# Optimization experiments

Measured on AMD Instinct MI355X. Metric: run time of the kernel, lower is better.

Reference implementation:

```python
import jax, jax.numpy as jnp
import numpy as np

D = 1024
H = 8          # MHA fallback num_heads
DH = D // H
DFF = 4096     # mlp_ratio * hidden_size
EPS = 1e-6


def _ln(x, g, b):
    mu = jnp.mean(x, axis=-1, keepdims=True)
    var = jnp.mean((x - mu) ** 2, axis=-1, keepdims=True)
    return (x - mu) * jax.lax.rsqrt(var + EPS) * g + b


def setup_inputs() -> dict:
    key = jax.random.key(0)
    ks = jax.random.split(key, 16)
    s = 0.02
    return {
        "x": jax.random.normal(ks[0], (8, 1024, D), jnp.float32),
        "c": jax.random.normal(ks[1], (8, D), jnp.float32),
        # Mamba-block (attention fallback) params
        "m_ada_w": jax.random.normal(ks[2], (D, 3 * D), jnp.float32) * s,
        "m_ada_b": jnp.zeros((3 * D,), jnp.float32),
        "m_norm_g": jnp.ones((D,), jnp.float32),
        "m_norm_b": jnp.zeros((D,), jnp.float32),
        "in_proj_w": jax.random.normal(ks[3], (3 * D, D), jnp.float32) * s,
        "in_proj_b": jnp.zeros((3 * D,), jnp.float32),
        "out_proj_w": jax.random.normal(ks[4], (D, D), jnp.float32) * s,
        "out_proj_b": jnp.zeros((D,), jnp.float32),
        # FeedForward-block params
        "f_ada_w": jax.random.normal(ks[5], (D, 3 * D), jnp.float32) * s,
        "f_ada_b": jnp.zeros((3 * D,), jnp.float32),
        "f_norm_g": jnp.ones((D,), jnp.float32),
        "f_norm_b": jnp.zeros((D,), jnp.float32),
        "w1": jax.random.normal(ks[6], (D, DFF), jnp.float32) * s,
        "b1": jnp.zeros((DFF,), jnp.float32),
        "w2": jax.random.normal(ks[7], (DFF, D), jnp.float32) * s,
        "b2": jnp.zeros((D,), jnp.float32),
    }


def reference(x, c, m_ada_w, m_ada_b, m_norm_g, m_norm_b, in_proj_w, in_proj_b,
              out_proj_w, out_proj_b, f_ada_w, f_ada_b, f_norm_g, f_norm_b,
              w1, b1, w2, b2):
    B, N, _ = x.shape
    # ---- MambaBlock (MHA fallback), dropout = identity (eval) ----
    mod = jax.nn.silu(c) @ m_ada_w + m_ada_b              # (B, 3D)
    shift, scale, gate = jnp.split(mod, 3, axis=-1)
    h = _ln(x, m_norm_g, m_norm_b)
    h = h * (1.0 + scale[:, None, :]) + shift[:, None, :]
    qkv = h @ in_proj_w.T + in_proj_b                      # (B, N, 3D)
    q, k, v = jnp.split(qkv, 3, axis=-1)
    q = q.reshape(B, N, H, DH)
    k = k.reshape(B, N, H, DH)
    v = v.reshape(B, N, H, DH)
    scores = jnp.einsum("bqhd,bkhd->bhqk", q, k) / np.sqrt(DH).astype(np.float32)
    attn = jax.nn.softmax(scores, axis=-1)
    o = jnp.einsum("bhqk,bkhd->bqhd", attn, v).reshape(B, N, D)
    o = o @ out_proj_w.T + out_proj_b
    x = x + gate[:, None, :] * o
    # ---- FeedForward block ----
    mod2 = jax.nn.silu(c) @ f_ada_w + f_ada_b
    shift2, scale2, gate2 = jnp.split(mod2, 3, axis=-1)
    h = _ln(x, f_norm_g, f_norm_b)
    h = h * (1.0 + scale2[:, None, :]) + shift2[:, None, :]
    h = jax.nn.gelu(h @ w1 + b1, approximate=False) @ w2 + b2
    return x + gate2[:, None, :] * h
```

## Files before the change

kernel.cpp:

```cpp
#include <hip/hip_runtime.h>

typedef __bf16 bf16x8 __attribute__((ext_vector_type(8)));
typedef float f32x4 __attribute__((ext_vector_type(4)));

__device__ __forceinline__ unsigned short f2bf(float f) {
    unsigned int u = __float_as_uint(f);
    unsigned int r = (u + 0x7FFFu + ((u >> 16) & 1u)) >> 16;
    return (unsigned short)r;
}

__device__ __forceinline__ void gload16(const void* g, void* l) {
    __builtin_amdgcn_global_load_lds(
        (const __attribute__((address_space(1))) unsigned int*)g,
        (__attribute__((address_space(3))) unsigned int*)l, 16, 0, 0);
}

__device__ __forceinline__ void barrier_raw() {
    asm volatile("" ::: "memory");
    __builtin_amdgcn_s_barrier();
    asm volatile("" ::: "memory");
}

__device__ __forceinline__ void vmwait0() {
    asm volatile("s_waitcnt vmcnt(0)" ::: "memory");
}

__device__ __forceinline__ float gelu_fast(float u) {
    float z = 1.595769122f * u + 0.071354816f * u * u * u;
    return u / (1.f + __expf(-z));
}

__global__ __launch_bounds__(256) void f2b4(const float* __restrict__ in,
                                            unsigned short* __restrict__ out) {
    size_t i = ((size_t)blockIdx.x * 256 + threadIdx.x) * 4;
    float4 v = *(const float4*)(in + i);
    ushort4 o;
    o.x = f2bf(v.x); o.y = f2bf(v.y); o.z = f2bf(v.z); o.w = f2bf(v.w);
    *(ushort4*)(out + i) = o;
}

__global__ __launch_bounds__(256) void transpose_f2b(const float* __restrict__ in,
                                                     unsigned short* __restrict__ out,
                                                     int R, int C) {
    __shared__ float tile[32][33];
    int r0 = blockIdx.y * 32, c0 = blockIdx.x * 32;
    int tx = threadIdx.x & 31, ty = threadIdx.x >> 5;
#pragma unroll
    for (int i = 0; i < 4; i++) {
        int r = ty + i * 8;
        tile[r][tx] = in[(size_t)(r0 + r) * C + c0 + tx];
    }
    __syncthreads();
#pragma unroll
    for (int i = 0; i < 4; i++) {
        int r = ty + i * 8;
        out[(size_t)(c0 + r) * R + r0 + tx] = f2bf(tile[tx][r]);
    }
}

__global__ __launch_bounds__(256) void transpose_v(const unsigned short* __restrict__ qkv,
                                                   unsigned short* __restrict__ vt) {
    __shared__ unsigned short tile[32][33];
    int head = blockIdx.z;
    int b = head >> 3;
    int n0 = blockIdx.x * 32, d0 = blockIdx.y * 32;
    int tx = threadIdx.x & 31, ty = threadIdx.x >> 5;
    const unsigned short* src = qkv + (size_t)(b * 1024) * 3072 + 2048 + (head & 7) * 128;
#pragma unroll
    for (int i = 0; i < 4; i++) {
        int n = ty + i * 8;
        tile[n][tx] = src[(size_t)(n0 + n) * 3072 + d0 + tx];
    }
    __syncthreads();
#pragma unroll
    for (int i = 0; i < 4; i++) {
        int d = ty + i * 8;
        vt[((size_t)head * 128 + d0 + d) * 1024 + n0 + tx] = tile[tx][d];
    }
}

__global__ __launch_bounds__(256) void ada_mod_part(const float* __restrict__ c,
                                                    const float* __restrict__ W,
                                                    float* __restrict__ partial) {
    __shared__ float sc[8 * 64];
    int kc = blockIdx.y * 64;
    for (int i = threadIdx.x; i < 512; i += 256) {
        int b = i >> 6, k = i & 63;
        float cv = c[b * 1024 + kc + k];
        sc[i] = cv / (1.f + __expf(-cv));
    }
    __syncthreads();
    int j = blockIdx.x * 256 + threadIdx.x;
    float acc[8] = {0, 0, 0, 0, 0, 0, 0, 0};
    for (int k = 0; k < 64; k++) {
        float w = W[(size_t)(kc + k) * 3072 + j];
#pragma unroll
        for (int b = 0; b < 8; b++) acc[b] += sc[b * 64 + k] * w;
    }
#pragma unroll
    for (int b = 0; b < 8; b++) partial[((size_t)blockIdx.y * 8 + b) * 3072 + j] = acc[b];
}

__global__ __launch_bounds__(256) void ada_reduce(const float* __restrict__ partial,
                                                  const float* __restrict__ bias,
                                                  float* __restrict__ out) {
    int idx = blockIdx.x * 256 + threadIdx.x;
    int b = idx / 3072;
    int jj = idx - b * 3072;
    float s = bias[jj];
#pragma unroll
    for (int ch = 0; ch < 16; ch++) s += partial[((size_t)ch * 8 + b) * 3072 + jj];
    out[idx] = s;
}

__global__ __launch_bounds__(256) void ln_mod_kernel(const float* __restrict__ x,
                                                     const float* __restrict__ gamma,
                                                     const float* __restrict__ beta,
                                                     const float* __restrict__ mods,
                                                     unsigned short* __restrict__ out) {
    int row = blockIdx.x;
    int b = row >> 10;
    float4 v = ((const float4*)(x + (size_t)row * 1024))[threadIdx.x];
    float s = v.x + v.y + v.z + v.w;
    float s2 = v.x * v.x + v.y * v.y + v.z * v.z + v.w * v.w;
#pragma unroll
    for (int d = 1; d < 64; d <<= 1) { s += __shfl_xor(s, d); s2 += __shfl_xor(s2, d); }
    __shared__ float red[8];
    int lane = threadIdx.x & 63, wid = threadIdx.x >> 6;
    if (lane == 0) { red[wid] = s; red[4 + wid] = s2; }
    __syncthreads();
    float S = red[0] + red[1] + red[2] + red[3];
    float S2 = red[4] + red[5] + red[6] + red[7];
    float mu = S * (1.f / 1024.f);
    float var = S2 * (1.f / 1024.f) - mu * mu;
    float rs = rsqrtf(var + 1e-6f);
    const float* mrow = mods + b * 3072;
    int j0 = threadIdx.x * 4;
    float hv[4] = {v.x, v.y, v.z, v.w};
    ushort4 o;
    unsigned short* op = (unsigned short*)&o;
#pragma unroll
    for (int i = 0; i < 4; i++) {
        int j = j0 + i;
        float hh = (hv[i] - mu) * rs * gamma[j] + beta[j];
        hh = hh * (1.f + mrow[1024 + j]) + mrow[j];
        op[i] = f2bf(hh);
    }
    *(ushort4*)(out + (size_t)row * 1024 + j0) = o;
}

template <int NF, int EP>
__global__ __launch_bounds__(512, 2) void gemm256(const unsigned short* __restrict__ A,
                                                  const unsigned short* __restrict__ Bt,
                                                  int N, int K, int nx,
                                                  const float* __restrict__ bias,
                                                  const float* __restrict__ xres,
                                                  const float* __restrict__ mods,
                                                  float* __restrict__ outf,
                                                  unsigned short* __restrict__ outb) {
    constexpr int BROWS = NF * 64;
    extern __shared__ __align__(16) char smem[];
    __bf16* AsB = (__bf16*)smem;
    __bf16* BsB = AsB + 2 * 256 * 64;

    int tid = threadIdx.x, lane = tid & 63, wid = tid >> 6;
    int wr = wid >> 2, wc = wid & 3;
    int t = lane & 15, g = lane >> 4;
    int xk = (t & 7) * 8;

    int nwg = gridDim.x;
    int chunk = nwg >> 3;
    int swz = (blockIdx.x & 7) * chunk + (blockIdx.x >> 3);
    int bx = swz % nx, by = swz / nx;
    int rowA0 = by * 256, colB0 = bx * BROWS;

    int rin = tid >> 3;
    int cblk = tid & 7;
    int scol = (cblk ^ (rin & 7)) * 8;

    auto stageA = [&](int nb, int half, int kt1) {
        int k0 = kt1 << 6;
        int r0 = half * 128 + rin;
        gload16(A + (size_t)(rowA0 + r0) * K + k0 + scol,
                (void*)(AsB + nb * (256 * 64) + r0 * 64 + cblk * 8));
        int r1 = r0 + 64;
        gload16(A + (size_t)(rowA0 + r1) * K + k0 + scol,
                (void*)(AsB + nb * (256 * 64) + r1 * 64 + cblk * 8));
    };
    auto stageB4 = [&](int nb, int half, int kt1) {
        int k0 = kt1 << 6;
        int r0 = half * 128 + rin;
        gload16(Bt + (size_t)(colB0 + r0) * K + k0 + scol,
                (void*)(BsB + nb * (BROWS * 64) + r0 * 64 + cblk * 8));
        int r1 = r0 + 64;
        gload16(Bt + (size_t)(colB0 + r1) * K + k0 + scol,
                (void*)(BsB + nb * (BROWS * 64) + r1 * 64 + cblk * 8));
    };
    auto stageB2 = [&](int nb, int half, int kt1) {
        int k0 = kt1 << 6;
        int r0 = half * 64 + rin;
        gload16(Bt + (size_t)(colB0 + r0) * K + k0 + scol,
                (void*)(BsB + nb * (BROWS * 64) + r0 * 64 + cblk * 8));
    };

    f32x4 acc[8][NF];
#pragma unroll
    for (int m = 0; m < 8; m++)
#pragma unroll
        for (int n = 0; n < NF; n++) acc[m][n] = (f32x4){0.f, 0.f, 0.f, 0.f};

    stageA(0, 0, 0); stageA(0, 1, 0);
    if constexpr (NF == 4) { stageB4(0, 0, 0); stageB4(0, 1, 0); }
    else                   { stageB2(0, 0, 0); stageB2(0, 1, 0); }
    vmwait0();
    barrier_raw();

    int NT = K >> 6;
#pragma unroll 1
    for (int kt = 0; kt < NT; ++kt) {
        const __bf16* Ac = AsB + (kt & 1) * (256 * 64);
        const __bf16* Bc = BsB + (kt & 1) * (BROWS * 64);
        int nb = (kt & 1) ^ 1;
        bool more = (kt + 1) < NT;

        auto LDA = [&](int m, int ks) -> bf16x8 {
            return *(const bf16x8*)(Ac + (wr * 128 + m * 16 + t) * 64 + ((ks * 32 + g * 8) ^ xk));
        };
        auto LDB = [&](int n, int ks) -> bf16x8 {
            return *(const bf16x8*)(Bc + (wc * (NF * 16) + n * 16 + t) * 64 + ((ks * 32 + g * 8) ^ xk));
        };

        if constexpr (NF == 4) {
            bf16x8 aF[4][2], bLo[2][2], bHi[2][2];
#pragma unroll
            for (int m = 0; m < 4; m++) { aF[m][0] = LDA(m, 0); aF[m][1] = LDA(m, 1); }
#pragma unroll
            for (int n = 0; n < 2; n++) { bLo[n][0] = LDB(n, 0); bLo[n][1] = LDB(n, 1); }
            if (more) stageA(nb, 0, kt + 1);
            barrier_raw();
            __builtin_amdgcn_s_setprio(1);
#pragma unroll
            for (int m = 0; m < 4; m++)
#pragma unroll
                for (int n = 0; n < 2; n++)
#pragma unroll
                    for (int ks = 0; ks < 2; ks++)
                        acc[m][n] = __builtin_amdgcn_mfma_f32_16x16x32_bf16(aF[m][ks], bLo[n][ks], acc[m][n], 0, 0, 0);
            __builtin_amdgcn_s_setprio(0);
            barrier_raw();
#pragma unroll
            for (int n = 0; n < 2; n++) { bHi[n][0] = LDB(n + 2, 0); bHi[n][1] = LDB(n + 2, 1); }
            if (more) stageA(nb, 1, kt + 1);
            barrier_raw();
            __builtin_amdgcn_s_setprio(1);
#pragma unroll
            for (int m = 0; m < 4; m++)
#pragma unroll
                for (int n = 0; n < 2; n++)
#pragma unroll
                    for (int ks = 0; ks < 2; ks++)
                        acc[m][n + 2] = __builtin_amdgcn_mfma_f32_16x16x32_bf16(aF[m][ks], bHi[n][ks], acc[m][n + 2], 0, 0, 0);
            __builtin_amdgcn_s_setprio(0);
            barrier_raw();
            bf16x8 aH[4][2];
#pragma unroll
            for (int m = 0; m < 4; m++) { aH[m][0] = LDA(m + 4, 0); aH[m][1] = LDA(m + 4, 1); }
            if (more) stageB4(nb, 0, kt + 1);
            barrier_raw();
            __builtin_amdgcn_s_setprio(1);
#pragma unroll
            for (int m = 0; m < 4; m++)
#pragma unroll
                for (int n = 0; n < 2; n++)
#pragma unroll
                    for (int ks = 0; ks < 2; ks++)
                        acc[m + 4][n + 2] = __builtin_amdgcn_mfma_f32_16x16x32_bf16(aH[m][ks], bHi[n][ks], acc[m + 4][n + 2], 0, 0, 0);
            __builtin_amdgcn_s_setprio(0);
            barrier_raw();
            if (more) stageB4(nb, 1, kt + 1);
            __builtin_amdgcn_s_setprio(1);
#pragma unroll
            for (int m = 0; m < 4; m++)
#pragma unroll
                for (int n = 0; n < 2; n++)
#pragma unroll
                    for (int ks = 0; ks < 2; ks++)
                        acc[m + 4][n] = __builtin_amdgcn_mfma_f32_16x16x32_bf16(aH[m][ks], bLo[n][ks], acc[m + 4][n], 0, 0, 0);
            __builtin_amdgcn_s_setprio(0);
            vmwait0();
            barrier_raw();
        } else {
            bf16x8 aF[4][2], bF[2][2];
#pragma unroll
            for (int m = 0; m < 4; m++) { aF[m][0] = LDA(m, 0); aF[m][1] = LDA(m, 1); }
#pragma unroll
            for (int n = 0; n < 2; n++) { bF[n][0] = LDB(n, 0); bF[n][1] = LDB(n, 1); }
            if (more) { stageA(nb, 0, kt + 1); stageB2(nb, 0, kt + 1); }
            barrier_raw();
            __builtin_amdgcn_s_setprio(1);
#pragma unroll
            for (int m = 0; m < 4; m++)
#pragma unroll
                for (int n = 0; n < 2; n++)
#pragma unroll
                    for (int ks = 0; ks < 2; ks++)
                        acc[m][n] = __builtin_amdgcn_mfma_f32_16x16x32_bf16(aF[m][ks], bF[n][ks], acc[m][n], 0, 0, 0);
            __builtin_amdgcn_s_setprio(0);
            barrier_raw();
            bf16x8 aH[4][2];
#pragma unroll
            for (int m = 0; m < 4; m++) { aH[m][0] = LDA(m + 4, 0); aH[m][1] = LDA(m + 4, 1); }
            if (more) { stageA(nb, 1, kt + 1); stageB2(nb, 1, kt + 1); }
            barrier_raw();
            __builtin_amdgcn_s_setprio(1);
#pragma unroll
            for (int m = 0; m < 4; m++)
#pragma unroll
                for (int n = 0; n < 2; n++)
#pragma unroll
                    for (int ks = 0; ks < 2; ks++)
                        acc[m + 4][n] = __builtin_amdgcn_mfma_f32_16x16x32_bf16(aH[m][ks], bF[n][ks], acc[m + 4][n], 0, 0, 0);
            __builtin_amdgcn_s_setprio(0);
            vmwait0();
            barrier_raw();
        }
    }

    int row0 = rowA0 + wr * 128, col0 = colB0 + wc * (NF * 16);
#pragma unroll
    for (int m = 0; m < 8; m++)
#pragma unroll
        for (int n = 0; n < NF; n++) {
            int col = col0 + n * 16 + t;
#pragma unroll
            for (int r = 0; r < 4; r++) {
                int row = row0 + m * 16 + g * 4 + r;
                float v = acc[m][n][r];
                if (EP == 0) {
                    outb[(size_t)row * N + col] = f2bf(v + bias[col]);
                } else if (EP == 1) {
                    int bb = row >> 10;
                    float gt = mods[bb * 3072 + 2048 + col];
                    outf[(size_t)row * 1024 + col] =
                        xres[(size_t)row * 1024 + col] + gt * (v + bias[col]);
                } else if (EP == 2) {
                    outb[(size_t)row * N + col] = f2bf(gelu_fast(v + bias[col]));
                } else {
                    int bb = row >> 10;
                    float gt = mods[bb * 3072 + 2048 + col];
                    outf[(size_t)row * 1024 + col] += gt * (v + bias[col]);
                }
            }
        }
}

__global__ __launch_bounds__(256) void attn_kernel(const unsigned short* __restrict__ qkv,
                                                   const unsigned short* __restrict__ vt,
                                                   unsigned short* __restrict__ o) {
    __shared__ __align__(16) __bf16 Ks[64 * 128];
    __shared__ __align__(16) __bf16 Vts[128 * 64];
    __shared__ __align__(16) __bf16 Pl[4][16][72];
    int bid = blockIdx.x;
    int logical = (bid & 7) * 128 + (bid >> 3);
    int q0 = (logical & 15) * 64;
    int bh = logical >> 4;
    int b = bh >> 3, h = bh & 7;
    int tid = threadIdx.x, lane = tid & 63, w = tid >> 6;
    int t = lane & 15, g = lane >> 4;
    int swzt = (t & 7) << 4;

    const unsigned short* qbase = qkv + (size_t)(b * 1024) * 3072 + h * 128;
    int qrow = q0 + w * 16 + t;
    bf16x8 qf[4];
#pragma unroll
    for (int ks = 0; ks < 4; ks++)
        qf[ks] = *(const bf16x8*)(qbase + (size_t)qrow * 3072 + ks * 32 + g * 8);

    f32x4 Oa[8];
#pragma unroll
    for (int n = 0; n < 8; n++) Oa[n] = (f32x4){0.f, 0.f, 0.f, 0.f};
    float m_r[4] = {-1e30f, -1e30f, -1e30f, -1e30f};
    float l_r[4] = {0.f, 0.f, 0.f, 0.f};
    const float scale = 0.08838834764831845f;

    int krow = tid >> 4;
    int ksrc = (((tid & 15) * 16) ^ ((krow & 7) << 4)) >> 1;
    int vrow = tid >> 3;
    int vsrc = (((tid & 7) * 16) ^ ((vrow & 7) << 4)) >> 1;
    const unsigned short* vtg = vt + (size_t)bh * 128 * 1024;

    for (int kv0 = 0; kv0 < 1024; kv0 += 64) {
        const unsigned short* kb = qkv + (size_t)(b * 1024 + kv0) * 3072 + 1024 + h * 128;
#pragma unroll
        for (int cc = 0; cc < 4; cc++) {
            gload16(kb + (size_t)(cc * 16 + krow) * 3072 + ksrc, (void*)&Ks[cc * 2048 + tid * 8]);
            gload16(vtg + (size_t)(cc * 32 + vrow) * 1024 + kv0 + vsrc, (void*)&Vts[cc * 2048 + tid * 8]);
        }
        __syncthreads();

        f32x4 Sa[4];
#pragma unroll
        for (int n = 0; n < 4; n++) Sa[n] = (f32x4){0.f, 0.f, 0.f, 0.f};
#pragma unroll
        for (int ks = 0; ks < 4; ks++) {
#pragma unroll
            for (int n = 0; n < 4; n++) {
                bf16x8 kf = *(const bf16x8*)&Ks[(n * 16 + t) * 128 + (((ks * 64 + g * 16) ^ swzt) >> 1)];
                Sa[n] = __builtin_amdgcn_mfma_f32_16x16x32_bf16(qf[ks], kf, Sa[n], 0, 0, 0);
            }
        }
#pragma unroll
        for (int r = 0; r < 4; r++) {
            float mx = fmaxf(fmaxf(Sa[0][r], Sa[1][r]), fmaxf(Sa[2][r], Sa[3][r])) * scale;
#pragma unroll
            for (int d = 1; d < 16; d <<= 1) mx = fmaxf(mx, __shfl_xor(mx, d));
            float mn = fmaxf(m_r[r], mx);
            float alpha = __expf(m_r[r] - mn);
            m_r[r] = mn;
            float rs = 0.f;
#pragma unroll
            for (int n = 0; n < 4; n++) {
                float p = __expf(Sa[n][r] * scale - mn);
                Pl[w][g * 4 + r][n * 16 + t] = (__bf16)p;
                rs += p;
            }
#pragma unroll
            for (int d = 1; d < 16; d <<= 1) rs += __shfl_xor(rs, d);
            l_r[r] = l_r[r] * alpha + rs;
#pragma unroll
            for (int n2 = 0; n2 < 8; n2++) Oa[n2][r] *= alpha;
        }
#pragma unroll
        for (int ks2 = 0; ks2 < 2; ks2++) {
            bf16x8 pa = *(const bf16x8*)&Pl[w][t][ks2 * 32 + g * 8];
#pragma unroll
            for (int n2 = 0; n2 < 8; n2++) {
                bf16x8 vf = *(const bf16x8*)&Vts[(n2 * 16 + t) * 64 + (((ks2 * 64 + g * 16) ^ swzt) >> 1)];
                Oa[n2] = __builtin_amdgcn_mfma_f32_16x16x32_bf16(pa, vf, Oa[n2], 0, 0, 0);
            }
        }
        __syncthreads();
    }

#pragma unroll
    for (int r = 0; r < 4; r++) {
        float inv = 1.f / l_r[r];
        int orow = q0 + w * 16 + g * 4 + r;
#pragma unroll
        for (int n2 = 0; n2 < 8; n2++)
            o[(size_t)(b * 1024 + orow) * 1024 + h * 128 + n2 * 16 + t] = f2bf(Oa[n2][r] * inv);
    }
}

extern "C" void kernel_launch(void* const* d_in, const int* in_sizes, int n_in,
                              void* d_out, int out_size, void* d_ws, size_t ws_size,
                              hipStream_t stream) {
    const float* x          = (const float*)d_in[0];
    const float* c          = (const float*)d_in[1];
    const float* m_ada_w    = (const float*)d_in[2];
    const float* m_ada_b    = (const float*)d_in[3];
    const float* m_norm_g   = (const float*)d_in[4];
    const float* m_norm_b   = (const float*)d_in[5];
    const float* in_proj_w  = (const float*)d_in[6];
    const float* in_proj_b  = (const float*)d_in[7];
    const float* out_proj_w = (const float*)d_in[8];
    const float* out_proj_b = (const float*)d_in[9];
    const float* f_ada_w    = (const float*)d_in[10];
    const float* f_ada_b    = (const float*)d_in[11];
    const float* f_norm_g   = (const float*)d_in[12];
    const float* f_norm_b   = (const float*)d_in[13];
    const float* w1         = (const float*)d_in[14];
    const float* b1         = (const float*)d_in[15];
    const float* w2         = (const float*)d_in[16];
    const float* b2         = (const float*)d_in[17];
    float* out = (float*)d_out;
    char* ws = (char*)d_ws;

    unsigned short* Wq   = (unsigned short*)(ws + 0);
    unsigned short* Wo   = (unsigned short*)(ws + 6291456);
    unsigned short* vt   = (unsigned short*)(ws + 8388608);
    unsigned short* W1t  = (unsigned short*)(ws + 8388608);
    unsigned short* W2t  = (unsigned short*)(ws + 16777216);
    float*          modm = (float*)(ws + 25165824);
    float*          modf = (float*)(ws + 25264128);
    unsigned short* hbuf = (unsigned short*)(ws + 25362432);
    float*          part = (float*)(ws + 25362432);
    float*          part2= (float*)(ws + 25362432 + 2097152);
    unsigned short* qkv  = (unsigned short*)(ws + 42139648);
    unsigned short* obuf = (unsigned short*)(ws + 92471296);
    unsigned short* h2   = (unsigned short*)(ws + 42139648);

    hipFuncSetAttribute((const void*)&gemm256<4, 0>, hipFuncAttributeMaxDynamicSharedMemorySize, 131072);
    hipFuncSetAttribute((const void*)&gemm256<4, 2>, hipFuncAttributeMaxDynamicSharedMemorySize, 131072);
    hipFuncSetAttribute((const void*)&gemm256<2, 1>, hipFuncAttributeMaxDynamicSharedMemorySize, 98304);
    hipFuncSetAttribute((const void*)&gemm256<2, 3>, hipFuncAttributeMaxDynamicSharedMemorySize, 98304);

    hipLaunchKernelGGL(ada_mod_part, dim3(12, 16), dim3(256), 0, stream, c, m_ada_w, part);
    hipLaunchKernelGGL(ada_mod_part, dim3(12, 16), dim3(256), 0, stream, c, f_ada_w, part2);
    hipLaunchKernelGGL(ada_reduce, dim3(96), dim3(256), 0, stream, part, m_ada_b, modm);
    hipLaunchKernelGGL(ada_reduce, dim3(96), dim3(256), 0, stream, part2, f_ada_b, modf);

    hipLaunchKernelGGL(f2b4, dim3(3072), dim3(256), 0, stream, in_proj_w, Wq);
    hipLaunchKernelGGL(f2b4, dim3(1024), dim3(256), 0, stream, out_proj_w, Wo);

    hipLaunchKernelGGL(ln_mod_kernel, dim3(8192), dim3(256), 0, stream, x, m_norm_g, m_norm_b, modm, hbuf);
    hipLaunchKernelGGL(HIP_KERNEL_NAME(gemm256<4, 0>), dim3(384), dim3(512), 131072, stream,
                       hbuf, Wq, 3072, 1024, 12, in_proj_b, (const float*)nullptr,
                       (const float*)nullptr, (float*)nullptr, qkv);
    hipLaunchKernelGGL(transpose_v, dim3(32, 4, 64), dim3(256), 0, stream, qkv, vt);
    hipLaunchKernelGGL(attn_kernel, dim3(1024), dim3(256), 0, stream, qkv, vt, obuf);
    hipLaunchKernelGGL(HIP_KERNEL_NAME(gemm256<2, 1>), dim3(256), dim3(512), 98304, stream,
                       obuf, Wo, 1024, 1024, 8, out_proj_b, x, modm, out, (unsigned short*)nullptr);

    hipLaunchKernelGGL(transpose_f2b, dim3(128, 32), dim3(256), 0, stream, w1, W1t, 1024, 4096);
    hipLaunchKernelGGL(transpose_f2b, dim3(32, 128), dim3(256), 0, stream, w2, W2t, 4096, 1024);

    hipLaunchKernelGGL(ln_mod_kernel, dim3(8192), dim3(256), 0, stream, out, f_norm_g, f_norm_b, modf, hbuf);
    hipLaunchKernelGGL(HIP_KERNEL_NAME(gemm256<4, 2>), dim3(512), dim3(512), 131072, stream,
                       hbuf, W1t, 4096, 1024, 16, b1, (const float*)nullptr,
                       (const float*)nullptr, (float*)nullptr, h2);
    hipLaunchKernelGGL(HIP_KERNEL_NAME(gemm256<2, 3>), dim3(256), dim3(512), 98304, stream,
                       h2, W2t, 1024, 4096, 8, b2, (const float*)nullptr, modf, out,
                       (unsigned short*)nullptr);
}
```

Baseline: 434.1 us.

## Double-buffer attention K/V tiles and keep P in registers via transposed S

The attention kernel now uses 512-thread blocks covering 128 query rows, with double-buffered K/V tiles in dynamic shared memory, so the next tile's global-to-LDS loads overlap the current tile's compute. S is computed transposed (K as the A operand), which lets each lane own one query column and do its softmax reduction with two cross-group shuffles. P is converted to the MFMA A-operand layout through lane shuffles instead of a round trip through the LDS P buffer. MFMA sections are wrapped in s_setprio hints. In exchange it doubles LDS per block and adds extra shuffle and select traffic in the inner loop.

New measurement: 392.7 us. -9.5%, faster.

```diff
diff --git a/kernel.cpp b/kernel.cpp
--- a/kernel.cpp
+++ b/kernel.cpp
@@ -354,16 +354,17 @@
         }
 }
 
-__global__ __launch_bounds__(256) void attn_kernel(const unsigned short* __restrict__ qkv,
-                                                   const unsigned short* __restrict__ vt,
-                                                   unsigned short* __restrict__ o) {
-    __shared__ __align__(16) __bf16 Ks[64 * 128];
-    __shared__ __align__(16) __bf16 Vts[128 * 64];
-    __shared__ __align__(16) __bf16 Pl[4][16][72];
+__global__ __launch_bounds__(512, 4) void attn_kernel(const unsigned short* __restrict__ qkv,
+                                                      const unsigned short* __restrict__ vt,
+                                                      unsigned short* __restrict__ o) {
+    extern __shared__ __align__(16) char asmem[];
+    __bf16* Ks = (__bf16*)asmem;
+    __bf16* Vts = Ks + 2 * 64 * 128;
+
     int bid = blockIdx.x;
-    int logical = (bid & 7) * 128 + (bid >> 3);
-    int q0 = (logical & 15) * 64;
-    int bh = logical >> 4;
+    int logical = (bid & 7) * 64 + (bid >> 3);
+    int q0 = (logical & 7) * 128;
+    int bh = logical >> 3;
     int b = bh >> 3, h = bh & 7;
     int tid = threadIdx.x, lane = tid & 63, w = tid >> 6;
     int t = lane & 15, g = lane >> 4;
@@ -379,8 +380,7 @@
     f32x4 Oa[8];
 #pragma unroll
     for (int n = 0; n < 8; n++) Oa[n] = (f32x4){0.f, 0.f, 0.f, 0.f};
-    float m_r[4] = {-1e30f, -1e30f, -1e30f, -1e30f};
-    float l_r[4] = {0.f, 0.f, 0.f, 0.f};
+    float m_r = -1e30f, l_r = 0.f;
     const float scale = 0.08838834764831845f;
 
     int krow = tid >> 4;
@@ -389,62 +389,115 @@
     int vsrc = (((tid & 7) * 16) ^ ((vrow & 7) << 4)) >> 1;
     const unsigned short* vtg = vt + (size_t)bh * 128 * 1024;
 
-    for (int kv0 = 0; kv0 < 1024; kv0 += 64) {
+    auto stage = [&](int buf, int kv0) {
         const unsigned short* kb = qkv + (size_t)(b * 1024 + kv0) * 3072 + 1024 + h * 128;
 #pragma unroll
-        for (int cc = 0; cc < 4; cc++) {
-            gload16(kb + (size_t)(cc * 16 + krow) * 3072 + ksrc, (void*)&Ks[cc * 2048 + tid * 8]);
-            gload16(vtg + (size_t)(cc * 32 + vrow) * 1024 + kv0 + vsrc, (void*)&Vts[cc * 2048 + tid * 8]);
-        }
-        __syncthreads();
-
-        f32x4 Sa[4];
-#pragma unroll
-        for (int n = 0; n < 4; n++) Sa[n] = (f32x4){0.f, 0.f, 0.f, 0.f};
+        for (int cc = 0; cc < 2; cc++) {
+            gload16(kb + (size_t)(cc * 32 + krow) * 3072 + ksrc,
+                    (void*)(Ks + buf * 8192 + cc * 4096 + tid * 8));
+            gload16(vtg + (size_t)(cc * 64 + vrow) * 1024 + kv0 + vsrc,
+                    (void*)(Vts + buf * 8192 + cc * 4096 + tid * 8));
+        }
+    };
+
+    stage(0, 0);
+    vmwait0();
+    barrier_raw();
+
+#pragma unroll 1
+    for (int tile = 0; tile < 16; ++tile) {
+        int cur = tile & 1;
+        bool more = tile < 15;
+        if (more) stage(cur ^ 1, (tile + 1) * 64);
+        const __bf16* Kc = Ks + cur * 8192;
+        const __bf16* Vc = Vts + cur * 8192;
+
+        f32x4 St[4];
+#pragma unroll
+        for (int n = 0; n < 4; n++) St[n] = (f32x4){0.f, 0.f, 0.f, 0.f};
+        __builtin_amdgcn_s_setprio(1);
 #pragma unroll
         for (int ks = 0; ks < 4; ks++) {
 #pragma unroll
             for (int n = 0; n < 4; n++) {
-                bf16x8 kf = *(const bf16x8*)&Ks[(n * 16 + t) * 128 + (((ks * 64 + g * 16) ^ swzt) >> 1)];
-                Sa[n] = __builtin_amdgcn_mfma_f32_16x16x32_bf16(qf[ks], kf, Sa[n], 0, 0, 0);
+                bf16x8 kf = *(const bf16x8*)&Kc[(n * 16 + t) * 128 + (((ks * 64 + g * 16) ^ swzt) >> 1)];
+                St[n] = __builtin_amdgcn_mfma_f32_16x16x32_bf16(kf, qf[ks], St[n], 0, 0, 0);
             }
         }
+        __builtin_amdgcn_s_setprio(0);
+
+        float mx = -1e30f;
+#pragma unroll
+        for (int n = 0; n < 4; n++)
+#pragma unroll
+            for (int r = 0; r < 4; r++) mx = fmaxf(mx, St[n][r]);
+        mx *= scale;
+        mx = fmaxf(mx, __shfl_xor(mx, 16));
+        mx = fmaxf(mx, __shfl_xor(mx, 32));
+        float mn = fmaxf(m_r, mx);
+        float alpha = __expf(m_r - mn);
+        m_r = mn;
+        float p[4][4];
+        float rs = 0.f;
+#pragma unroll
+        for (int n = 0; n < 4; n++)
+#pragma unroll
+            for (int r = 0; r < 4; r++) {
+                float pv = __expf(St[n][r] * scale - mn);
+                p[n][r] = pv;
+                rs += pv;
+            }
+        rs += __shfl_xor(rs, 16);
+        rs += __shfl_xor(rs, 32);
+        l_r = l_r * alpha + rs;
+
+        unsigned P01[4], P23[4];
+#pragma unroll
+        for (int n = 0; n < 4; n++) {
+            P01[n] = (unsigned)f2bf(p[n][0]) | ((unsigned)f2bf(p[n][1]) << 16);
+            P23[n] = (unsigned)f2bf(p[n][2]) | ((unsigned)f2bf(p[n][3]) << 16);
+        }
+
 #pragma unroll
         for (int r = 0; r < 4; r++) {
-            float mx = fmaxf(fmaxf(Sa[0][r], Sa[1][r]), fmaxf(Sa[2][r], Sa[3][r])) * scale;
-#pragma unroll
-            for (int d = 1; d < 16; d <<= 1) mx = fmaxf(mx, __shfl_xor(mx, d));
-            float mn = fmaxf(m_r[r], mx);
-            float alpha = __expf(m_r[r] - mn);
-            m_r[r] = mn;
-            float rs = 0.f;
-#pragma unroll
-            for (int n = 0; n < 4; n++) {
-                float p = __expf(Sa[n][r] * scale - mn);
-                Pl[w][g * 4 + r][n * 16 + t] = (__bf16)p;
-                rs += p;
+            float ar = __shfl(alpha, (lane & 48) + g * 4 + r);
+#pragma unroll
+            for (int n2 = 0; n2 < 8; n2++) Oa[n2][r] *= ar;
+        }
+
+#pragma unroll
+        for (int ks2 = 0; ks2 < 2; ks2++) {
+            int e = ks2 * 2, od = ks2 * 2 + 1;
+            unsigned s16a = (g < 2) ? P01[e] : P01[od];
+            unsigned s16b = (g < 2) ? P23[e] : P23[od];
+            unsigned s32a = (g & 1) ? P01[e] : P01[od];
+            unsigned s32b = (g & 1) ? P23[e] : P23[od];
+            unsigned s48a = (g >= 2) ? P01[e] : P01[od];
+            unsigned s48b = (g >= 2) ? P23[e] : P23[od];
+            unsigned r16a = __shfl_xor(s16a, 16), r16b = __shfl_xor(s16b, 16);
+            unsigned r32a = __shfl_xor(s32a, 32), r32b = __shfl_xor(s32b, 32);
+            unsigned r48a = __shfl_xor(s48a, 48), r48b = __shfl_xor(s48b, 48);
+            union { unsigned u[4]; bf16x8 v; } pa;
+            pa.u[0] = (g == 0) ? P01[e] : (g == 1) ? r48a : (g == 2) ? r32a : r16a;
+            pa.u[1] = (g == 0) ? P23[e] : (g == 1) ? r48b : (g == 2) ? r32b : r16b;
+            pa.u[2] = (g == 0) ? r16a : (g == 1) ? r32a : (g == 2) ? r48a : P01[od];
+            pa.u[3] = (g == 0) ? r16b : (g == 1) ? r32b : (g == 2) ? r48b : P23[od];
+            __builtin_amdgcn_s_setprio(1);
+#pragma unroll
+            for (int n2 = 0; n2 < 8; n2++) {
+                bf16x8 vf = *(const bf16x8*)&Vc[(n2 * 16 + t) * 64 + (((ks2 * 64 + g * 16) ^ swzt) >> 1)];
+                Oa[n2] = __builtin_amdgcn_mfma_f32_16x16x32_bf16(pa.v, vf, Oa[n2], 0, 0, 0);
             }
-#pragma unroll
-            for (int d = 1; d < 16; d <<= 1) rs += __shfl_xor(rs, d);
-            l_r[r] = l_r[r] * alpha + rs;
-#pragma unroll
-            for (int n2 = 0; n2 < 8; n2++) Oa[n2][r] *= alpha;
-        }
-#pragma unroll
-        for (int ks2 = 0; ks2 < 2; ks2++) {
-            bf16x8 pa = *(const bf16x8*)&Pl[w][t][ks2 * 32 + g * 8];
-#pragma unroll
-            for (int n2 = 0; n2 < 8; n2++) {
-                bf16x8 vf = *(const bf16x8*)&Vts[(n2 * 16 + t) * 64 + (((ks2 * 64 + g * 16) ^ swzt) >> 1)];
-                Oa[n2] = __builtin_amdgcn_mfma_f32_16x16x32_bf16(pa, vf, Oa[n2], 0, 0, 0);
-            }
-        }
-        __syncthreads();
+            __builtin_amdgcn_s_setprio(0);
+        }
+
+        if (more) { vmwait0(); barrier_raw(); }
     }
 
 #pragma unroll
     for (int r = 0; r < 4; r++) {
-        float inv = 1.f / l_r[r];
+        float lq = __shfl(l_r, (lane & 48) + g * 4 + r);
+        float inv = 1.f / lq;
         int orow = q0 + w * 16 + g * 4 + r;
 #pragma unroll
         for (int n2 = 0; n2 < 8; n2++)
@@ -494,6 +547,7 @@
     hipFuncSetAttribute((const void*)&gemm256<4, 2>, hipFuncAttributeMaxDynamicSharedMemorySize, 131072);
     hipFuncSetAttribute((const void*)&gemm256<2, 1>, hipFuncAttributeMaxDynamicSharedMemorySize, 98304);
     hipFuncSetAttribute((const void*)&gemm256<2, 3>, hipFuncAttributeMaxDynamicSharedMemorySize, 98304);
+    hipFuncSetAttribute((const void*)&attn_kernel, hipFuncAttributeMaxDynamicSharedMemorySize, 65536);
 
     hipLaunchKernelGGL(ada_mod_part, dim3(12, 16), dim3(256), 0, stream, c, m_ada_w, part);
     hipLaunchKernelGGL(ada_mod_part, dim3(12, 16), dim3(256), 0, stream, c, f_ada_w, part2);
@@ -508,7 +562,7 @@
                        hbuf, Wq, 3072, 1024, 12, in_proj_b, (const float*)nullptr,
                        (const float*)nullptr, (float*)nullptr, qkv);
     hipLaunchKernelGGL(transpose_v, dim3(32, 4, 64), dim3(256), 0, stream, qkv, vt);
-    hipLaunchKernelGGL(attn_kernel, dim3(1024), dim3(256), 0, stream, qkv, vt, obuf);
+    hipLaunchKernelGGL(attn_kernel, dim3(512), dim3(512), 65536, stream, qkv, vt, obuf);
     hipLaunchKernelGGL(HIP_KERNEL_NAME(gemm256<2, 1>), dim3(256), dim3(512), 98304, stream,
                        obuf, Wo, 1024, 1024, 8, out_proj_b, x, modm, out, (unsigned short*)nullptr);
 
```
